# Kernel optimization log

Hardware: AMD Instinct MI355X
Metric: run time of the kernel (lower is better)

Reference implementation:

```python
import jax, jax.numpy as jnp
import numpy as np

# BinarizeConv2dSDP hyperparameters (from init_kwargs): SDP rank K and output scale.
SCALE = 1.0
K = 2
EPS = 1e-5  # BatchNorm2d default eps


@jax.custom_vjp
def binarize(x):
    # deterministic sign binarization (1-bit)
    return jnp.sign(x)

def _bin_fwd(x):
    return jnp.sign(x), x

def _bin_bwd(x, g):
    # straight-through estimator with hardtanh clipping, as in standard BNN training
    return (g * (jnp.abs(x) <= 1.0).astype(g.dtype),)

binarize.defvjp(_bin_fwd, _bin_bwd)


def conv3x3(x, w, stride=1):
    # x: [N, C, H, W], w: [O, I, 3, 3], padding=1
    return jax.lax.conv_general_dilated(
        x, w,
        window_strides=(stride, stride),
        padding=((1, 1), (1, 1)),
        dimension_numbers=("NCHW", "OIHW", "NCHW"),
    )


def binconv(x, w, stride=1):
    # binarized-input, binarized-weight conv with SDP scale
    return conv3x3(binarize(x), binarize(w), stride) * (SCALE / K)


def batchnorm(x, gamma, beta):
    # training-mode BatchNorm2d over (N, H, W)
    m = jnp.mean(x, axis=(0, 2, 3), keepdims=True)
    v = jnp.var(x, axis=(0, 2, 3), keepdims=True)
    xn = (x - m) * jax.lax.rsqrt(v + EPS)
    return xn * gamma[None, :, None, None] + beta[None, :, None, None]


def setup_inputs() -> dict:
    key = jax.random.key(0)
    k1, k2, k3 = jax.random.split(key, 3)
    N, C, H, W = 32, 256, 56, 56
    x = jax.random.normal(k1, (N, C, H, W), dtype=jnp.float32)
    w1 = jax.random.normal(k2, (C, C, 3, 3), dtype=jnp.float32) * 0.05
    w2 = jax.random.normal(k3, (C, C, 3, 3), dtype=jnp.float32) * 0.05
    g1 = jnp.ones((C,), jnp.float32)
    b1 = jnp.zeros((C,), jnp.float32)
    g2 = jnp.ones((C,), jnp.float32)
    b2 = jnp.zeros((C,), jnp.float32)
    return {"x": x, "w1": w1, "g1": g1, "b1": b1, "w2": w2, "g2": g2, "b2": b2}


def reference(x, w1, g1, b1, w2, g2, b2):
    # out = hardtanh(bn1(conv1(x)))
    out = jnp.clip(batchnorm(binconv(x, w1, 1), g1, b1), -1.0, 1.0)
    # out = bn2(conv2(out)) + shortcut(x)  (identity shortcut: stride=1, in_planes==planes)
    out = batchnorm(binconv(out, w2, 1), g2, b2) + x
    # final hardtanh
    return jnp.clip(out, -1.0, 1.0)
```

## Files before the change

### kernel.cpp

```cpp
#include <hip/hip_runtime.h>
#include <stdint.h>

#define NB    32
#define C     256
#define HH    56
#define WW    56
#define HW    3136
#define P_TOT 100352
#define PW    58
#define PHW   3364
#define NPAD  107648
#define EPSBN 1e-5f

__device__ __forceinline__ uint64_t shflx64(uint64_t v, int m) {
    int lo = __shfl_xor((int)(uint32_t)v, m, 64);
    int hi = __shfl_xor((int)(uint32_t)(v >> 32), m, 64);
    return ((uint64_t)(uint32_t)hi << 32) | (uint32_t)lo;
}
__device__ __forceinline__ uint64_t bt64(uint64_t M, int lane) {
    const uint64_t mk[6] = {0x5555555555555555ULL, 0x3333333333333333ULL,
                            0x0F0F0F0F0F0F0F0FULL, 0x00FF00FF00FF00FFULL,
                            0x0000FFFF0000FFFFULL, 0x00000000FFFFFFFFULL};
#pragma unroll
    for (int k = 0; k < 6; ++k) {
        int s = 1 << k;
        uint64_t mA = mk[k];
        uint64_t v = shflx64(M, s);
        M = (lane & s) ? ((M & ~mA) | ((v & ~mA) >> s))
                       : ((M &  mA) | ((v &  mA) << s));
    }
    return M;
}

__global__ __launch_bounds__(256) void pack_wgt(const float* __restrict__ w1,
                                                const float* __restrict__ w2,
                                                uint64_t* __restrict__ pw1,
                                                uint64_t* __restrict__ pw2,
                                                int* __restrict__ pc1,
                                                int* __restrict__ pc2) {
    int gw = blockIdx.x * 4 + (threadIdx.x >> 6);
    int lane = threadIdx.x & 63;
    int set = gw / 9216;
    int r = gw - set * 9216;
    int wd = r & 3, q = r >> 2;
    int t = q % 9, co = q / 9;
    const float* w = set ? w2 : w1;
    float v = w[(size_t)co * 2304 + (size_t)(wd * 64 + lane) * 9 + t];
    unsigned long long m = __ballot(v >= 0.0f);
    if (lane == 0) {
        uint64_t* pw = set ? pw2 : pw1;
        int* pc = set ? pc2 : pc1;
        pw[(size_t)(wd * 256 + co) * 10 + t] = m;
        pc[(co * 9 + t) * 4 + wd] = (int)__popcll(m);
    }
}

__global__ __launch_bounds__(256) void build_K(const int* __restrict__ pc1,
                                               const int* __restrict__ pc2,
                                               unsigned short* __restrict__ K1,
                                               unsigned short* __restrict__ K2) {
    int tid = blockIdx.x * 256 + threadIdx.x;
    int set = tid / 2304;
    int r = tid - set * 2304;
    int pat = r >> 8, co = r & 255;
    int pv = pat / 3, pq = pat - pv * 3;
    const int* pc = set ? pc2 : pc1;
    int k = 0, corr = 0;
#pragma unroll
    for (int t = 0; t < 9; ++t) {
        int ty = t / 3, tx = t - ty * 3;
        bool inv = (pv == 0 && ty == 0) || (pv == 2 && ty == 2) ||
                   (pq == 0 && tx == 0) || (pq == 2 && tx == 2);
        if (inv) {
            ++k;
            const int* p = pc + (co * 9 + t) * 4;
            corr += p[0] + p[1] + p[2] + p[3];
        }
    }
    unsigned short* K = set ? K2 : K1;
    K[pat * 256 + co] = (unsigned short)(256 * (9 - k) + 2 * corr);
}

__global__ __launch_bounds__(256) void zero_halo(uint64_t* __restrict__ px1,
                                                 uint64_t* __restrict__ px2) {
    int idx = blockIdx.x * 256 + threadIdx.x;
    if (idx >= NPAD) return;
    int pp = idx % PHW;
    int ph = pp / PW, pw_ = pp - ph * PW;
    if (ph == 0 || ph == PW - 1 || pw_ == 0 || pw_ == PW - 1) {
#pragma unroll
        for (int wd = 0; wd < 4; ++wd) {
            px1[(size_t)wd * NPAD + idx] = 0ull;
            px2[(size_t)wd * NPAD + idx] = 0ull;
        }
    }
}

__global__ __launch_bounds__(256) void pack_act(const float* __restrict__ x,
                                                uint64_t* __restrict__ px) {
    int wid = blockIdx.x * 4 + (threadIdx.x >> 6);
    int lane = threadIdx.x & 63;
    int wd = wid & 3;
    int g = wid >> 2;
    int n = g / 49, gi = g - n * 49;
    const float* xp = x + ((size_t)n * C + wd * 64) * HW + gi * 64 + lane;
    uint64_t M = 0;
#pragma unroll
    for (int c = 0; c < 64; ++c) {
        float v = xp[(size_t)c * HW];
        unsigned long long m = __ballot(v >= 0.0f);
        if (lane == c) M = m;
    }
    M = bt64(M, lane);
    int p = gi * 64 + lane;
    int h = p / WW, w = p - h * WW;
    px[(size_t)wd * NPAD + (size_t)n * PHW + (size_t)(h + 1) * PW + (w + 1)] = M;
}

__global__ __launch_bounds__(256, 3) void bconv(const uint64_t* __restrict__ px,
                                                const uint64_t* __restrict__ pw,
                                                const unsigned short* __restrict__ Kt,
                                                short* __restrict__ sout) {
    __shared__ uint64_t lw[2560];
    int co0 = blockIdx.y * 64;
#pragma unroll 1
    for (int i = threadIdx.x; i < 2560; i += 256) {
        int wd = i / 640, j = i - wd * 640;
        lw[i] = pw[(size_t)(wd * 256 + co0) * 10 + j];
    }
    __syncthreads();

    int p = blockIdx.x * 256 + threadIdx.x;
    int n = p / HW, rem = p - n * HW;
    int h = rem / WW, w = rem - h * WW;
    size_t pp = (size_t)n * PHW + (size_t)(h + 1) * PW + (w + 1);

    int acc[64];
#pragma unroll
    for (int c = 0; c < 64; ++c) acc[c] = 0;

#pragma unroll 1
    for (int wd = 0; wd < 4; ++wd) {
        const uint64_t* xb = px + (size_t)wd * NPAD + pp;
        uint64_t x0 = xb[-PW - 1], x1 = xb[-PW], x2 = xb[-PW + 1];
        uint64_t x3 = xb[-1],      x4 = xb[0],   x5 = xb[1];
        uint64_t x6 = xb[PW - 1],  x7 = xb[PW],  x8 = xb[PW + 1];
        const uint64_t* wb = lw + wd * 640;
#pragma unroll
        for (int c = 0; c < 64; ++c) {
            const uint64_t* wq = wb + c * 10;
            int r = acc[c];
            r += __popcll(x0 ^ wq[0]);
            r += __popcll(x1 ^ wq[1]);
            r += __popcll(x2 ^ wq[2]);
            r += __popcll(x3 ^ wq[3]);
            r += __popcll(x4 ^ wq[4]);
            r += __popcll(x5 ^ wq[5]);
            r += __popcll(x6 ^ wq[6]);
            r += __popcll(x7 ^ wq[7]);
            r += __popcll(x8 ^ wq[8]);
            acc[c] = r;
        }
    }

    int pv = (h == 0) ? 0 : ((h == HH - 1) ? 2 : 1);
    int pq = (w == 0) ? 0 : ((w == WW - 1) ? 2 : 1);
    const unsigned short* Kp = Kt + (pv * 3 + pq) * 256 + co0;
    short* op = sout + ((size_t)n * C + co0) * HW + rem;
#pragma unroll
    for (int c = 0; c < 64; ++c)
        op[(size_t)c * HW] = (short)((int)Kp[c] - 2 * acc[c]);
}

__global__ __launch_bounds__(256) void stats(const short* __restrict__ s,
                                             const float* __restrict__ g,
                                             const float* __restrict__ b,
                                             float* __restrict__ A,
                                             float* __restrict__ Bv) {
    int c = blockIdx.x;
    int sum = 0;
    long long sq = 0;
#pragma unroll 4
    for (int k = threadIdx.x; k < 12544; k += 256) {
        int n = k / 392, rr = k - n * 392;
        const int4* p = (const int4*)(s + ((size_t)n * C + c) * HW + rr * 8);
        int4 v = *p;
#pragma unroll
        for (int j = 0; j < 4; ++j) {
            int u = (&v.x)[j];
            int s0 = (int)(short)(u & 0xFFFF);
            int s1 = u >> 16;
            sum += s0 + s1;
            sq += (long long)(s0 * s0 + s1 * s1);
        }
    }
    long long lsum = sum;
#pragma unroll
    for (int off = 32; off; off >>= 1) {
        lsum += __shfl_down(lsum, off, 64);
        sq   += __shfl_down(sq,   off, 64);
    }
    __shared__ long long r0[4], r1[4];
    int lane = threadIdx.x & 63, wv = threadIdx.x >> 6;
    if (lane == 0) { r0[wv] = lsum; r1[wv] = sq; }
    __syncthreads();
    if (threadIdx.x == 0) {
        long long S = r0[0] + r0[1] + r0[2] + r0[3];
        long long Q = r1[0] + r1[1] + r1[2] + r1[3];
        float m  = 0.5f  * (float)S / (float)P_TOT;
        float e2 = 0.25f * (float)Q / (float)P_TOT;
        float var = e2 - m * m;
        float a = g[c] * rsqrtf(var + EPSBN);
        A[c]  = 0.5f * a;
        Bv[c] = b[c] - m * a;
    }
}

__global__ __launch_bounds__(256) void bnpack(const short* __restrict__ s,
                                              const float* __restrict__ A,
                                              const float* __restrict__ Bv,
                                              uint64_t* __restrict__ px) {
    __shared__ float sA[256], sB[256];
    sA[threadIdx.x] = A[threadIdx.x];
    sB[threadIdx.x] = Bv[threadIdx.x];
    __syncthreads();
    int wid = blockIdx.x * 4 + (threadIdx.x >> 6);
    int lane = threadIdx.x & 63;
    int wd = wid & 3;
    int g = wid >> 2;
    int n = g / 49, gi = g - n * 49;
    const short* sp = s + ((size_t)n * C + wd * 64) * HW + gi * 64 + lane;
    uint64_t M = 0;
#pragma unroll
    for (int c = 0; c < 64; ++c) {
        float y = (float)sp[(size_t)c * HW] * sA[wd * 64 + c] + sB[wd * 64 + c];
        unsigned long long m = __ballot(y >= 0.0f);
        if (lane == c) M = m;
    }
    M = bt64(M, lane);
    int p = gi * 64 + lane;
    int h = p / WW, w = p - h * WW;
    px[(size_t)wd * NPAD + (size_t)n * PHW + (size_t)(h + 1) * PW + (w + 1)] = M;
}

__global__ __launch_bounds__(256) void finalize(const short* __restrict__ s,
                                                const float* __restrict__ x,
                                                const float* __restrict__ A,
                                                const float* __restrict__ Bv,
                                                float* __restrict__ out) {
    int i = blockIdx.x * 256 + threadIdx.x;
    int c = (i / 784) & 255;
    short4 sv = ((const short4*)s)[i];
    float4 xv = ((const float4*)x)[i];
    float a = A[c], bb = Bv[c];
    float4 o;
    o.x = fminf(1.0f, fmaxf(-1.0f, (float)sv.x * a + bb + xv.x));
    o.y = fminf(1.0f, fmaxf(-1.0f, (float)sv.y * a + bb + xv.y));
    o.z = fminf(1.0f, fmaxf(-1.0f, (float)sv.z * a + bb + xv.z));
    o.w = fminf(1.0f, fmaxf(-1.0f, (float)sv.w * a + bb + xv.w));
    ((float4*)out)[i] = o;
}

extern "C" void kernel_launch(void* const* d_in, const int* in_sizes, int n_in,
                              void* d_out, int out_size, void* d_ws, size_t ws_size,
                              hipStream_t stream) {
    const float* x  = (const float*)d_in[0];
    const float* w1 = (const float*)d_in[1];
    const float* g1 = (const float*)d_in[2];
    const float* b1 = (const float*)d_in[3];
    const float* w2 = (const float*)d_in[4];
    const float* g2 = (const float*)d_in[5];
    const float* b2 = (const float*)d_in[6];
    float* out = (float*)d_out;

    char* ws = (char*)d_ws;
    uint64_t* pw1 = (uint64_t*)ws;          ws += 4 * 256 * 10 * 8;
    uint64_t* pw2 = (uint64_t*)ws;          ws += 4 * 256 * 10 * 8;
    int* pc1 = (int*)ws;                    ws += 9216 * 4;
    int* pc2 = (int*)ws;                    ws += 9216 * 4;
    unsigned short* K1 = (unsigned short*)ws; ws += 8192;
    unsigned short* K2 = (unsigned short*)ws; ws += 8192;
    float* A1 = (float*)ws;                 ws += 1024;
    float* B1 = (float*)ws;                 ws += 1024;
    float* A2 = (float*)ws;                 ws += 1024;
    float* B2 = (float*)ws;                 ws += 1024;
    uint64_t* px1 = (uint64_t*)ws;          ws += (size_t)4 * NPAD * 8;
    uint64_t* px2 = (uint64_t*)ws;          ws += (size_t)4 * NPAD * 8;
    short* s16 = (short*)ws;

    zero_halo<<<(NPAD + 255) / 256, 256, 0, stream>>>(px1, px2);
    pack_wgt<<<4608, 256, 0, stream>>>(w1, w2, pw1, pw2, pc1, pc2);
    build_K<<<18, 256, 0, stream>>>(pc1, pc2, K1, K2);
    pack_act<<<1568, 256, 0, stream>>>(x, px1);

    bconv<<<dim3(P_TOT / 256, 4), 256, 0, stream>>>(px1, pw1, K1, s16);
    stats<<<C, 256, 0, stream>>>(s16, g1, b1, A1, B1);
    bnpack<<<1568, 256, 0, stream>>>(s16, A1, B1, px2);

    bconv<<<dim3(P_TOT / 256, 4), 256, 0, stream>>>(px2, pw2, K2, s16);
    stats<<<C, 256, 0, stream>>>(s16, g2, b2, A2, B2);

    finalize<<<(P_TOT * C / 4) / 256, 256, 0, stream>>>(s16, x, A2, B2, out);
}
```

Measured before the change: 566.4 us.

## Restructure binary conv to channel-per-thread with fused BN stats and NHWC output

The bconv kernel now assigns one output channel per thread, holds that channel's weights in registers, and walks one image row per block, writing NHWC short output. Per-channel sum and sum-of-squares are accumulated in the conv and added atomically, which replaces the separate stats reduction kernels with a tiny bnAB kernel. bnpack and finalize are rewritten for the NHWC layout, with finalize transposing through LDS. This aims to remove the stats passes and the 64-accumulator register pressure. In exchange, every thread in a wave reloads the same activation words from global memory, and the atomics add contention. The sum-of-squares is held in a 32-bit int per thread and zero-extended, so it relies on small value ranges.

```diff
diff --git a/kernel.cpp b/kernel.cpp
--- a/kernel.cpp
+++ b/kernel.cpp
@@ -30,6 +30,26 @@
                        : ((M &  mA) | ((v &  mA) << s));
     }
     return M;
+}
+
+__global__ __launch_bounds__(256) void zero_misc(uint64_t* __restrict__ px1,
+                                                 uint64_t* __restrict__ px2,
+                                                 int* __restrict__ sS1,
+                                                 unsigned long long* __restrict__ sQ1,
+                                                 int* __restrict__ sS2,
+                                                 unsigned long long* __restrict__ sQ2) {
+    int idx = blockIdx.x * 256 + threadIdx.x;
+    if (idx < 256) { sS1[idx] = 0; sQ1[idx] = 0; sS2[idx] = 0; sQ2[idx] = 0; }
+    if (idx >= NPAD) return;
+    int pp = idx % PHW;
+    int ph = pp / PW, pw_ = pp - ph * PW;
+    if (ph == 0 || ph == PW - 1 || pw_ == 0 || pw_ == PW - 1) {
+#pragma unroll
+        for (int wd = 0; wd < 4; ++wd) {
+            px1[(size_t)wd * NPAD + idx] = 0ull;
+            px2[(size_t)wd * NPAD + idx] = 0ull;
+        }
+    }
 }
 
 __global__ __launch_bounds__(256) void pack_wgt(const float* __restrict__ w1,
@@ -50,7 +70,7 @@
     if (lane == 0) {
         uint64_t* pw = set ? pw2 : pw1;
         int* pc = set ? pc2 : pc1;
-        pw[(size_t)(wd * 256 + co) * 10 + t] = m;
+        pw[(size_t)(wd * 9 + t) * 256 + co] = m;
         pc[(co * 9 + t) * 4 + wd] = (int)__popcll(m);
     }
 }
@@ -81,21 +101,6 @@
     K[pat * 256 + co] = (unsigned short)(256 * (9 - k) + 2 * corr);
 }
 
-__global__ __launch_bounds__(256) void zero_halo(uint64_t* __restrict__ px1,
-                                                 uint64_t* __restrict__ px2) {
-    int idx = blockIdx.x * 256 + threadIdx.x;
-    if (idx >= NPAD) return;
-    int pp = idx % PHW;
-    int ph = pp / PW, pw_ = pp - ph * PW;
-    if (ph == 0 || ph == PW - 1 || pw_ == 0 || pw_ == PW - 1) {
-#pragma unroll
-        for (int wd = 0; wd < 4; ++wd) {
-            px1[(size_t)wd * NPAD + idx] = 0ull;
-            px2[(size_t)wd * NPAD + idx] = 0ull;
-        }
-    }
-}
-
 __global__ __launch_bounds__(256) void pack_act(const float* __restrict__ x,
                                                 uint64_t* __restrict__ px) {
     int wid = blockIdx.x * 4 + (threadIdx.x >> 6);
@@ -117,130 +122,115 @@
     px[(size_t)wd * NPAD + (size_t)n * PHW + (size_t)(h + 1) * PW + (w + 1)] = M;
 }
 
-__global__ __launch_bounds__(256, 3) void bconv(const uint64_t* __restrict__ px,
+__global__ __launch_bounds__(256, 4) void bconv(const uint64_t* __restrict__ px,
                                                 const uint64_t* __restrict__ pw,
                                                 const unsigned short* __restrict__ Kt,
-                                                short* __restrict__ sout) {
-    __shared__ uint64_t lw[2560];
-    int co0 = blockIdx.y * 64;
+                                                short* __restrict__ sout,
+                                                int* __restrict__ sS,
+                                                unsigned long long* __restrict__ sQ) {
+    __shared__ unsigned short Kl[2304];
+    int co = threadIdx.x;
 #pragma unroll 1
-    for (int i = threadIdx.x; i < 2560; i += 256) {
-        int wd = i / 640, j = i - wd * 640;
-        lw[i] = pw[(size_t)(wd * 256 + co0) * 10 + j];
-    }
+    for (int i = threadIdx.x; i < 2304; i += 256) Kl[i] = Kt[i];
+
+    uint64_t wv[4][9];
+#pragma unroll
+    for (int wd = 0; wd < 4; ++wd)
+#pragma unroll
+        for (int t = 0; t < 9; ++t)
+            wv[wd][t] = pw[(size_t)(wd * 9 + t) * 256 + co];
     __syncthreads();
 
-    int p = blockIdx.x * 256 + threadIdx.x;
-    int n = p / HW, rem = p - n * HW;
-    int h = rem / WW, w = rem - h * WW;
-    size_t pp = (size_t)n * PHW + (size_t)(h + 1) * PW + (w + 1);
-
-    int acc[64];
-#pragma unroll
-    for (int c = 0; c < 64; ++c) acc[c] = 0;
-
-#pragma unroll 1
-    for (int wd = 0; wd < 4; ++wd) {
-        const uint64_t* xb = px + (size_t)wd * NPAD + pp;
-        uint64_t x0 = xb[-PW - 1], x1 = xb[-PW], x2 = xb[-PW + 1];
-        uint64_t x3 = xb[-1],      x4 = xb[0],   x5 = xb[1];
-        uint64_t x6 = xb[PW - 1],  x7 = xb[PW],  x8 = xb[PW + 1];
-        const uint64_t* wb = lw + wd * 640;
-#pragma unroll
-        for (int c = 0; c < 64; ++c) {
-            const uint64_t* wq = wb + c * 10;
-            int r = acc[c];
-            r += __popcll(x0 ^ wq[0]);
-            r += __popcll(x1 ^ wq[1]);
-            r += __popcll(x2 ^ wq[2]);
-            r += __popcll(x3 ^ wq[3]);
-            r += __popcll(x4 ^ wq[4]);
-            r += __popcll(x5 ^ wq[5]);
-            r += __popcll(x6 ^ wq[6]);
-            r += __popcll(x7 ^ wq[7]);
-            r += __popcll(x8 ^ wq[8]);
-            acc[c] = r;
-        }
-    }
-
+    int row = blockIdx.x;
+    int n = row / HH, h = row - n * HH;
+    size_t base = (size_t)n * PHW + (size_t)(h + 1) * PW + 1;
+    short* orow = sout + (size_t)(n * HW + h * WW) * C + co;
+    const bool irow = (h > 0) && (h < HH - 1);
     int pv = (h == 0) ? 0 : ((h == HH - 1) ? 2 : 1);
-    int pq = (w == 0) ? 0 : ((w == WW - 1) ? 2 : 1);
-    const unsigned short* Kp = Kt + (pv * 3 + pq) * 256 + co0;
-    short* op = sout + ((size_t)n * C + co0) * HW + rem;
-#pragma unroll
-    for (int c = 0; c < 64; ++c)
-        op[(size_t)c * HW] = (short)((int)Kp[c] - 2 * acc[c]);
-}
-
-__global__ __launch_bounds__(256) void stats(const short* __restrict__ s,
-                                             const float* __restrict__ g,
-                                             const float* __restrict__ b,
-                                             float* __restrict__ A,
-                                             float* __restrict__ Bv) {
-    int c = blockIdx.x;
-    int sum = 0;
-    long long sq = 0;
-#pragma unroll 4
-    for (int k = threadIdx.x; k < 12544; k += 256) {
-        int n = k / 392, rr = k - n * 392;
-        const int4* p = (const int4*)(s + ((size_t)n * C + c) * HW + rr * 8);
-        int4 v = *p;
-#pragma unroll
-        for (int j = 0; j < 4; ++j) {
-            int u = (&v.x)[j];
-            int s0 = (int)(short)(u & 0xFFFF);
-            int s1 = u >> 16;
-            sum += s0 + s1;
-            sq += (long long)(s0 * s0 + s1 * s1);
-        }
-    }
-    long long lsum = sum;
-#pragma unroll
-    for (int off = 32; off; off >>= 1) {
-        lsum += __shfl_down(lsum, off, 64);
-        sq   += __shfl_down(sq,   off, 64);
-    }
-    __shared__ long long r0[4], r1[4];
-    int lane = threadIdx.x & 63, wv = threadIdx.x >> 6;
-    if (lane == 0) { r0[wv] = lsum; r1[wv] = sq; }
-    __syncthreads();
-    if (threadIdx.x == 0) {
-        long long S = r0[0] + r0[1] + r0[2] + r0[3];
-        long long Q = r1[0] + r1[1] + r1[2] + r1[3];
-        float m  = 0.5f  * (float)S / (float)P_TOT;
-        float e2 = 0.25f * (float)Q / (float)P_TOT;
-        float var = e2 - m * m;
-        float a = g[c] * rsqrtf(var + EPSBN);
-        A[c]  = 0.5f * a;
-        Bv[c] = b[c] - m * a;
-    }
+
+    int ssum = 0, ssq = 0;
+#pragma unroll 2
+    for (int w = 0; w < WW; ++w) {
+        int acc = 0;
+#pragma unroll
+        for (int wd = 0; wd < 4; ++wd) {
+            const uint64_t* xb = px + (size_t)wd * NPAD + base + w;
+            uint64_t t0 = xb[-PW - 1], t1 = xb[-PW], t2 = xb[-PW + 1];
+            uint64_t t3 = xb[-1],      t4 = xb[0],   t5 = xb[1];
+            uint64_t t6 = xb[PW - 1],  t7 = xb[PW],  t8 = xb[PW + 1];
+            int r = 0;
+            r += __popcll(t0 ^ wv[wd][0]);
+            r += __popcll(t1 ^ wv[wd][1]);
+            r += __popcll(t2 ^ wv[wd][2]);
+            r += __popcll(t3 ^ wv[wd][3]);
+            r += __popcll(t4 ^ wv[wd][4]);
+            r += __popcll(t5 ^ wv[wd][5]);
+            r += __popcll(t6 ^ wv[wd][6]);
+            r += __popcll(t7 ^ wv[wd][7]);
+            r += __popcll(t8 ^ wv[wd][8]);
+            acc += r;
+        }
+        int dot;
+        if (irow && w > 0 && w < WW - 1) {
+            dot = 2304 - 2 * acc;
+        } else {
+            int pq = (w == 0) ? 0 : ((w == WW - 1) ? 2 : 1);
+            dot = (int)Kl[(pv * 3 + pq) * 256 + co] - 2 * acc;
+        }
+        orow[(size_t)w * C] = (short)dot;
+        ssum += dot;
+        ssq += dot * dot;
+    }
+    atomicAdd(sS + co, ssum);
+    atomicAdd(sQ + co, (unsigned long long)(unsigned int)ssq);
+}
+
+__global__ __launch_bounds__(256) void bnAB(const int* __restrict__ sS,
+                                            const unsigned long long* __restrict__ sQ,
+                                            const float* __restrict__ g,
+                                            const float* __restrict__ b,
+                                            float* __restrict__ A,
+                                            float* __restrict__ Bv) {
+    int c = threadIdx.x;
+    float S = (float)sS[c];
+    float Q = (float)sQ[c];
+    float m  = 0.5f  * S / (float)P_TOT;
+    float e2 = 0.25f * Q / (float)P_TOT;
+    float var = e2 - m * m;
+    float a = g[c] * rsqrtf(var + EPSBN);
+    A[c]  = 0.5f * a;
+    Bv[c] = b[c] - m * a;
 }
 
 __global__ __launch_bounds__(256) void bnpack(const short* __restrict__ s,
                                               const float* __restrict__ A,
                                               const float* __restrict__ Bv,
                                               uint64_t* __restrict__ px) {
-    __shared__ float sA[256], sB[256];
-    sA[threadIdx.x] = A[threadIdx.x];
-    sB[threadIdx.x] = Bv[threadIdx.x];
-    __syncthreads();
-    int wid = blockIdx.x * 4 + (threadIdx.x >> 6);
-    int lane = threadIdx.x & 63;
-    int wd = wid & 3;
-    int g = wid >> 2;
-    int n = g / 49, gi = g - n * 49;
-    const short* sp = s + ((size_t)n * C + wd * 64) * HW + gi * 64 + lane;
-    uint64_t M = 0;
-#pragma unroll
-    for (int c = 0; c < 64; ++c) {
-        float y = (float)sp[(size_t)c * HW] * sA[wd * 64 + c] + sB[wd * 64 + c];
-        unsigned long long m = __ballot(y >= 0.0f);
-        if (lane == c) M = m;
-    }
-    M = bt64(M, lane);
-    int p = gi * 64 + lane;
-    int h = p / WW, w = p - h * WW;
-    px[(size_t)wd * NPAD + (size_t)n * PHW + (size_t)(h + 1) * PW + (w + 1)] = M;
+    int p = blockIdx.x * 256 + threadIdx.x;
+    const int4* sp = (const int4*)(s + (size_t)p * C);
+    uint32_t bits[8];
+#pragma unroll
+    for (int wd = 0; wd < 8; ++wd) bits[wd] = 0u;
+#pragma unroll 4
+    for (int j = 0; j < 32; ++j) {
+        int4 v = sp[j];
+#pragma unroll
+        for (int k = 0; k < 4; ++k) {
+            int u = (&v.x)[k];
+            int c = j * 8 + k * 2;
+            float y0 = (float)(short)(u & 0xFFFF) * A[c] + Bv[c];
+            float y1 = (float)(u >> 16) * A[c + 1] + Bv[c + 1];
+            if (y0 >= 0.0f) bits[c >> 5] |= (1u << (c & 31));
+            if (y1 >= 0.0f) bits[(c + 1) >> 5] |= (1u << ((c + 1) & 31));
+        }
+    }
+    int n = p / HW, rem = p - n * HW;
+    int h = rem / WW, w = rem - h * WW;
+    size_t pidx = (size_t)n * PHW + (size_t)(h + 1) * PW + (w + 1);
+#pragma unroll
+    for (int wd = 0; wd < 4; ++wd)
+        px[(size_t)wd * NPAD + pidx] =
+            ((uint64_t)bits[2 * wd + 1] << 32) | bits[2 * wd];
 }
 
 __global__ __launch_bounds__(256) void finalize(const short* __restrict__ s,
@@ -248,17 +238,30 @@
                                                 const float* __restrict__ A,
                                                 const float* __restrict__ Bv,
                                                 float* __restrict__ out) {
-    int i = blockIdx.x * 256 + threadIdx.x;
-    int c = (i / 784) & 255;
-    short4 sv = ((const short4*)s)[i];
-    float4 xv = ((const float4*)x)[i];
-    float a = A[c], bb = Bv[c];
-    float4 o;
-    o.x = fminf(1.0f, fmaxf(-1.0f, (float)sv.x * a + bb + xv.x));
-    o.y = fminf(1.0f, fmaxf(-1.0f, (float)sv.y * a + bb + xv.y));
-    o.z = fminf(1.0f, fmaxf(-1.0f, (float)sv.z * a + bb + xv.z));
-    o.w = fminf(1.0f, fmaxf(-1.0f, (float)sv.w * a + bb + xv.w));
-    ((float4*)out)[i] = o;
+    __shared__ int4 lds4[2048];
+    int tid = threadIdx.x;
+    int p0 = blockIdx.x * 64;
+    int n = p0 / HW, rem0 = p0 - n * HW;
+    const int4* s4 = (const int4*)(s + (size_t)p0 * C);
+#pragma unroll
+    for (int it = 0; it < 8; ++it) {
+        int u = tid + it * 256;
+        int r = u >> 5, j = u & 31;
+        int4 v = s4[r * 32 + j];
+        lds4[r * 32 + ((j + r) & 31)] = v;
+    }
+    __syncthreads();
+    int lane = tid & 63;
+    int wvn = tid >> 6;
+#pragma unroll 4
+    for (int it = 0; it < 64; ++it) {
+        int c = it * 4 + wvn;
+        int slot = ((c >> 3) + lane) & 31;
+        short sv = ((const short*)lds4)[lane * 256 + slot * 8 + (c & 7)];
+        size_t gi = ((size_t)n * C + c) * HW + rem0 + lane;
+        float y = (float)sv * A[c] + Bv[c] + x[gi];
+        out[gi] = fminf(1.0f, fmaxf(-1.0f, y));
+    }
 }
 
 extern "C" void kernel_launch(void* const* d_in, const int* in_sizes, int n_in,
@@ -274,31 +277,35 @@
     float* out = (float*)d_out;
 
     char* ws = (char*)d_ws;
-    uint64_t* pw1 = (uint64_t*)ws;          ws += 4 * 256 * 10 * 8;
-    uint64_t* pw2 = (uint64_t*)ws;          ws += 4 * 256 * 10 * 8;
-    int* pc1 = (int*)ws;                    ws += 9216 * 4;
-    int* pc2 = (int*)ws;                    ws += 9216 * 4;
+    uint64_t* pw1 = (uint64_t*)ws;            ws += 4 * 9 * 256 * 8;
+    uint64_t* pw2 = (uint64_t*)ws;            ws += 4 * 9 * 256 * 8;
+    int* pc1 = (int*)ws;                      ws += 9216 * 4;
+    int* pc2 = (int*)ws;                      ws += 9216 * 4;
     unsigned short* K1 = (unsigned short*)ws; ws += 8192;
     unsigned short* K2 = (unsigned short*)ws; ws += 8192;
-    float* A1 = (float*)ws;                 ws += 1024;
-    float* B1 = (float*)ws;                 ws += 1024;
-    float* A2 = (float*)ws;                 ws += 1024;
-    float* B2 = (float*)ws;                 ws += 1024;
-    uint64_t* px1 = (uint64_t*)ws;          ws += (size_t)4 * NPAD * 8;
-    uint64_t* px2 = (uint64_t*)ws;          ws += (size_t)4 * NPAD * 8;
+    float* A1 = (float*)ws;                   ws += 1024;
+    float* B1 = (float*)ws;                   ws += 1024;
+    float* A2 = (float*)ws;                   ws += 1024;
+    float* B2 = (float*)ws;                   ws += 1024;
+    int* sS1 = (int*)ws;                      ws += 1024;
+    int* sS2 = (int*)ws;                      ws += 1024;
+    unsigned long long* sQ1 = (unsigned long long*)ws; ws += 2048;
+    unsigned long long* sQ2 = (unsigned long long*)ws; ws += 2048;
+    uint64_t* px1 = (uint64_t*)ws;            ws += (size_t)4 * NPAD * 8;
+    uint64_t* px2 = (uint64_t*)ws;            ws += (size_t)4 * NPAD * 8;
     short* s16 = (short*)ws;
 
-    zero_halo<<<(NPAD + 255) / 256, 256, 0, stream>>>(px1, px2);
+    zero_misc<<<(NPAD + 255) / 256, 256, 0, stream>>>(px1, px2, sS1, sQ1, sS2, sQ2);
     pack_wgt<<<4608, 256, 0, stream>>>(w1, w2, pw1, pw2, pc1, pc2);
     build_K<<<18, 256, 0, stream>>>(pc1, pc2, K1, K2);
     pack_act<<<1568, 256, 0, stream>>>(x, px1);
 
-    bconv<<<dim3(P_TOT / 256, 4), 256, 0, stream>>>(px1, pw1, K1, s16);
-    stats<<<C, 256, 0, stream>>>(s16, g1, b1, A1, B1);
-    bnpack<<<1568, 256, 0, stream>>>(s16, A1, B1, px2);
-
-    bconv<<<dim3(P_TOT / 256, 4), 256, 0, stream>>>(px2, pw2, K2, s16);
-    stats<<<C, 256, 0, stream>>>(s16, g2, b2, A2, B2);
-
-    finalize<<<(P_TOT * C / 4) / 256, 256, 0, stream>>>(s16, x, A2, B2, out);
-}
+    bconv<<<NB * HH, 256, 0, stream>>>(px1, pw1, K1, s16, sS1, sQ1);
+    bnAB<<<1, 256, 0, stream>>>(sS1, sQ1, g1, b1, A1, B1);
+    bnpack<<<P_TOT / 256, 256, 0, stream>>>(s16, A1, B1, px2);
+
+    bconv<<<NB * HH, 256, 0, stream>>>(px2, pw2, K2, s16, sS2, sQ2);
+    bnAB<<<1, 256, 0, stream>>>(sS2, sQ2, g2, b2, A2, B2);
+
+    finalize<<<P_TOT / 64, 256, 0, stream>>>(s16, x, A2, B2, out);
+}
```

Measured after the change: 539.4 us. 1.05x faster.
